# Kernel optimization log

Hardware: AMD Instinct MI355X
Metric: run time of the kernel (lower is better)

Reference implementation:

```python
import jax, jax.numpy as jnp
import numpy as np

LMAX, MMAX = 6, 2
C, COUT = 64, 64
E = 50000


def _perms():
    # l-primary coefficient order: for l in 0..lmax, m in -min(l,mmax)..min(l,mmax)
    lp = [(l, m) for l in range(LMAX + 1) for m in range(-min(l, MMAX), min(l, MMAX) + 1)]
    # m-primary order: m=0 block, then for each m>0: real (+m) block then imag (-m) block
    mp = [(l, 0) for l in range(LMAX + 1)]
    for m in range(1, MMAX + 1):
        mp += [(l, m) for l in range(m, LMAX + 1)]
        mp += [(l, -m) for l in range(m, LMAX + 1)]
    to_m = np.array([lp.index(p) for p in mp])   # gather: l-primary -> m-primary
    from_m = np.argsort(to_m)                    # inverse gather: m-primary -> l-primary
    return to_m, from_m

TO_M, FROM_M = _perms()


def setup_inputs() -> dict:
    key = jax.random.key(0)
    ks = jax.random.split(key, 6)
    sz0 = LMAX + 1                      # m_size[0] = 7
    in0 = sz0 * C                       # fc_m0 in_features = 448
    out0 = COUT * sz0                   # fc_m0 out_features = 448
    sz1, sz2 = LMAX, LMAX - 1           # m_size[1]=6, m_size[2]=5
    inp = {
        "x_embedding": jax.random.normal(ks[0], (E, len(TO_M), C), dtype=jnp.float32),
        "x_edge": jax.random.normal(ks[1], (E, 1), dtype=jnp.float32),
        "W0": jax.random.normal(ks[2], (out0, in0), dtype=jnp.float32) / np.sqrt(in0),
        "b0": jnp.zeros((out0,), dtype=jnp.float32),
        "W1": jax.random.normal(ks[3], (2 * COUT * sz1, sz1 * C), dtype=jnp.float32) / np.sqrt(2 * sz1 * C),
        "W2": jax.random.normal(ks[4], (2 * COUT * sz2, sz2 * C), dtype=jnp.float32) / np.sqrt(2 * sz2 * C),
    }
    return inp


def reference(x_embedding, x_edge, W0, b0, W1, W2):
    num_edges = x_embedding.shape[0]
    # _m_primary: permute coefficients to m-primary layout
    x = x_embedding[:, TO_M, :]                         # [E, 29, C]
    out = []
    # m = 0 path (fc_m0 with bias)
    sz0 = LMAX + 1
    x0 = x[:, :sz0, :].reshape(num_edges, sz0 * C)
    x0 = x0 @ W0.T + b0                                 # [E, sz0*COUT]
    out.append(x0.reshape(num_edges, sz0, COUT))
    # m = 1..mmax: SO2_m_Convolution (complex multiply structure)
    offset = sz0
    for m, Wm in zip(range(1, MMAX + 1), (W1, W2)):
        sz = LMAX - m + 1
        xm = x[:, offset:offset + 2 * sz, :].reshape(num_edges, 2, sz * C)
        y = jnp.einsum('enk,ok->eno', xm, Wm)           # [E, 2, 2*sz*COUT]
        half = sz * COUT
        x_r, x_i = y[..., :half], y[..., half:]
        x_m_r = x_r[:, 0:1] - x_i[:, 1:2]
        x_m_i = x_r[:, 1:2] + x_i[:, 0:1]
        xm_out = jnp.concatenate((x_m_r, x_m_i), axis=1)  # [E, 2, sz*COUT]
        out.append(xm_out.reshape(num_edges, 2 * sz, COUT))
        offset += 2 * sz
    out = jnp.concatenate(out, axis=1)                  # [E, 29, COUT] m-primary
    # _l_primary: back to l-primary layout
    return out[:, FROM_M, :]
```

## Files before the change

### kernel.cpp

```cpp
#include <hip/hip_runtime.h>
#include <hip/hip_bf16.h>

typedef __attribute__((ext_vector_type(8))) short short8;
typedef __attribute__((ext_vector_type(4))) float f32x4;

#define XSTRIDE 1856
#define CCH 64
#define OFF1 229376
#define OFF2 819200
#define WTOT 1228800

__constant__ int d_TO_M[29] = {0,2,6,11,16,21,26, 3,7,12,17,22,27, 1,5,10,15,20,25,
                               8,13,18,23,28, 4,9,14,19,24};

__device__ __forceinline__ short f2bf(float f) {
    __hip_bfloat16 h = __float2bfloat16(f);
    return __builtin_bit_cast(short, h);
}

__device__ __forceinline__ void load16_lds(const void* g, void* l) {
    __builtin_amdgcn_global_load_lds((const __attribute__((address_space(1))) unsigned int*)g,
                                     (__attribute__((address_space(3))) unsigned int*)l, 16, 0, 0);
}

__global__ __launch_bounds__(256) void prep_weights(const float* __restrict__ W0,
                                                    const float* __restrict__ W1,
                                                    const float* __restrict__ W2,
                                                    short* __restrict__ ws) {
    int idx = blockIdx.x * 256 + threadIdx.x;
    if (idx < OFF1) {
        ws[idx] = (idx < 448 * 448) ? f2bf(W0[idx]) : (short)0;
        return;
    }
    if (idx < OFF2) {
        int i = idx - OFF1;
        int n = i / 768, k = i % 768;
        int no = n / 384, ni = n % 384;
        int ki = k % 384;
        float v;
        if (no == (k / 384)) v =  W1[ni * 384 + ki];
        else if (no == 0)    v = -W1[(384 + ni) * 384 + ki];
        else                 v =  W1[(384 + ni) * 384 + ki];
        ws[idx] = f2bf(v);
        return;
    }
    if (idx < WTOT) {
        int i = idx - OFF2;
        int n = i / 640, k = i % 640;
        int no = n / 320, ni = n % 320;
        int ki = k % 320;
        float v;
        if (no == (k / 320)) v =  W2[ni * 320 + ki];
        else if (no == 0)    v = -W2[(320 + ni) * 320 + ki];
        else                 v =  W2[(320 + ni) * 320 + ki];
        ws[idx] = f2bf(v);
    }
}

__global__ __launch_bounds__(256, 2) void so2_gemm_f(const float* __restrict__ x,
                                                     const float* __restrict__ b0,
                                                     const short* __restrict__ wsW,
                                                     float* __restrict__ out,
                                                     int E, int nwg) {
    int orig = blockIdx.x;
    int q8 = nwg >> 3, r8 = nwg & 7;
    int xcd = orig & 7, pos = orig >> 3;
    int wgid = (xcd < r8 ? xcd * (q8 + 1) : r8 * (q8 + 1) + (xcd - r8) * q8) + pos;

    int etile = wgid / 15;
    int ncol  = wgid % 15;
    int blk, ntl;
    if (ncol < 4)       { blk = 0; ntl = ncol; }
    else if (ncol < 10) { blk = 1; ntl = ncol - 4; }
    else                { blk = 2; ntl = ncol - 10; }
    const int Kb     = (blk == 0) ? 448 : (blk == 1) ? 768 : 640;
    const int ksteps = Kb >> 5;
    const int kbase  = (blk == 0) ? 0 : (blk == 1) ? 7 : 19;
    const int nrows  = (blk == 0) ? 7 : (blk == 1) ? 12 : 10;
    const long woff  = (blk == 0) ? 0 : (blk == 1) ? (long)OFF1 : (long)OFF2;
    const short* Wb  = wsW + woff;
    const int n0 = ntl * 128;

    __shared__ float Af[3][128 * 32];
    __shared__ short Bf[2][128 * 32];

    const int tid  = threadIdx.x;
    const int w    = tid >> 6, lane = tid & 63;
    const int wr   = w >> 1,   wc   = w & 1;
    const int lrow = lane & 15, lk  = lane >> 4;
    const int ebase = etile * 128;

    const int lr = lane >> 3;
    const int ca = (lane & 7) ^ lr;
    const int rbq = lane >> 2;
    const int cb = (lane & 3) ^ ((lane >> 3) & 3);

    f32x4 acc[4][4] = {};

    auto stageA = [&](int kt, int pb) {
        int g = d_TO_M[kbase + (kt >> 1)];
        const float* src = x + (size_t)g * CCH + (kt & 1) * 32 + ca * 4;
#pragma unroll
        for (int j = 0; j < 4; ++j) {
            int rb = w * 32 + j * 8;
            int e = ebase + rb + lr;
            if (e >= E) e = E - 1;
            load16_lds(src + (size_t)e * XSTRIDE,
                       (char*)&Af[pb][rb * 32] + lane * 16);
        }
    };
    auto stageB = [&](int kt, int pb) {
        const short* src = Wb + (size_t)kt * 32 + cb * 8;
#pragma unroll
        for (int j = 0; j < 2; ++j) {
            int rb = w * 32 + j * 16;
            int n = n0 + rb + rbq;
            load16_lds(src + (size_t)n * Kb,
                       (char*)&Bf[pb][rb * 32] + lane * 16);
        }
    };
    auto compute = [&](int pa, int pbb) {
        short8 af[4], bf[4];
#pragma unroll
        for (int mf = 0; mf < 4; ++mf) {
            int r = wr * 64 + mf * 16 + lrow;
            int s0 = (2 * lk) ^ (lrow & 7);
            int s1 = (2 * lk + 1) ^ (lrow & 7);
            f32x4 lo = *(const f32x4*)&Af[pa][r * 32 + s0 * 4];
            f32x4 hi = *(const f32x4*)&Af[pa][r * 32 + s1 * 4];
            short8 v;
#pragma unroll
            for (int j = 0; j < 4; ++j) { v[j] = f2bf(lo[j]); v[4 + j] = f2bf(hi[j]); }
            af[mf] = v;
        }
#pragma unroll
        for (int nf = 0; nf < 4; ++nf) {
            int r = wc * 64 + nf * 16 + lrow;
            int s = lk ^ ((lrow >> 1) & 3);
            bf[nf] = *(const short8*)&Bf[pbb][r * 32 + s * 8];
        }
#pragma unroll
        for (int mf = 0; mf < 4; ++mf)
#pragma unroll
            for (int nf = 0; nf < 4; ++nf)
                acc[mf][nf] = __builtin_amdgcn_mfma_f32_16x16x32_bf16(af[mf], bf[nf], acc[mf][nf], 0, 0, 0);
    };

    stageA(0, 0);
    stageB(0, 0);
    stageA(1, 1);
    asm volatile("s_waitcnt vmcnt(4)" ::: "memory");
    __builtin_amdgcn_s_barrier();
    __builtin_amdgcn_sched_barrier(0);

    int pa = 0;
    for (int kt = 0; kt < ksteps; ++kt) {
        int pa1 = pa + 1; if (pa1 == 3) pa1 = 0;
        int pa2 = pa1 + 1; if (pa2 == 3) pa2 = 0;
        if (kt + 1 < ksteps) stageB(kt + 1, (kt + 1) & 1);
        __builtin_amdgcn_sched_barrier(0);
        if (kt + 2 < ksteps) stageA(kt + 2, pa2);
        compute(pa, kt & 1);
        if (kt + 2 < ksteps) {
            asm volatile("s_waitcnt vmcnt(4)" ::: "memory");
        } else if (kt + 1 < ksteps) {
            asm volatile("s_waitcnt vmcnt(0)" ::: "memory");
        }
        __builtin_amdgcn_s_barrier();
        __builtin_amdgcn_sched_barrier(0);
        pa = pa1;
    }

    int mrow_l = ntl * 2 + wc;
    if (mrow_l < nrows) {
        int lp = d_TO_M[kbase + mrow_l];
        float* op = out + (size_t)lp * CCH;
#pragma unroll
        for (int nf = 0; nf < 4; ++nf) {
            int c = nf * 16 + lrow;
            float bias = 0.f;
            if (blk == 0) bias = b0[mrow_l * 64 + c];
#pragma unroll
            for (int mf = 0; mf < 4; ++mf) {
                int e0 = ebase + wr * 64 + mf * 16 + lk * 4;
#pragma unroll
                for (int j = 0; j < 4; ++j) {
                    int e = e0 + j;
                    if (e < E) op[(size_t)e * XSTRIDE + c] = acc[mf][nf][j] + bias;
                }
            }
        }
    }
}

extern "C" void kernel_launch(void* const* d_in, const int* in_sizes, int n_in,
                              void* d_out, int out_size, void* d_ws, size_t ws_size,
                              hipStream_t stream) {
    const float* x_emb = (const float*)d_in[0];
    const float* W0 = (const float*)d_in[2];
    const float* b0 = (const float*)d_in[3];
    const float* W1 = (const float*)d_in[4];
    const float* W2 = (const float*)d_in[5];
    float* out = (float*)d_out;
    short* ws  = (short*)d_ws;

    const int E = in_sizes[0] / (29 * CCH);
    const int etiles = (E + 127) / 128;
    const int nwg = etiles * 15;

    prep_weights<<<(WTOT + 255) / 256, 256, 0, stream>>>(W0, W1, W2, ws);
    so2_gemm_f<<<nwg, 256, 0, stream>>>(x_emb, b0, (const short*)ws, out, E, nwg);
}
```

Before: 452.7 us.

## Keep weight stripe resident in LDS and stream activations directly from global

Replaces the pipelined 128x128 tiled GEMM with a kernel where each 512-thread block loads one 64-column weight stripe (the full K) into LDS once, then loops over four 512-edge groups. Activations are read straight from global memory into registers and converted to bf16, with no LDS staging or double buffering. The aim is to stop re-fetching weights for every edge tile and to drop the barrier-heavy multi-stage pipeline. In exchange, A loads are no longer software-pipelined, and each stripe re-reads the same activation rows across the 29 stripes, so activation reuse now relies on cache.

Result: slower. 662.4 us (+46.3%).

```diff
diff --git a/kernel.cpp b/kernel.cpp
--- a/kernel.cpp
+++ b/kernel.cpp
@@ -3,6 +3,7 @@
 
 typedef __attribute__((ext_vector_type(8))) short short8;
 typedef __attribute__((ext_vector_type(4))) float f32x4;
+typedef __attribute__((ext_vector_type(4))) unsigned int uint4v;
 
 #define XSTRIDE 1856
 #define CCH 64
@@ -10,17 +11,9 @@
 #define OFF2 819200
 #define WTOT 1228800
 
-__constant__ int d_TO_M[29] = {0,2,6,11,16,21,26, 3,7,12,17,22,27, 1,5,10,15,20,25,
-                               8,13,18,23,28, 4,9,14,19,24};
-
 __device__ __forceinline__ short f2bf(float f) {
     __hip_bfloat16 h = __float2bfloat16(f);
     return __builtin_bit_cast(short, h);
-}
-
-__device__ __forceinline__ void load16_lds(const void* g, void* l) {
-    __builtin_amdgcn_global_load_lds((const __attribute__((address_space(1))) unsigned int*)g,
-                                     (__attribute__((address_space(3))) unsigned int*)l, 16, 0, 0);
 }
 
 __global__ __launch_bounds__(256) void prep_weights(const float* __restrict__ W0,
@@ -57,140 +50,122 @@
     }
 }
 
-__global__ __launch_bounds__(256, 2) void so2_gemm_f(const float* __restrict__ x,
-                                                     const float* __restrict__ b0,
-                                                     const short* __restrict__ wsW,
-                                                     float* __restrict__ out,
-                                                     int E, int nwg) {
-    int orig = blockIdx.x;
-    int q8 = nwg >> 3, r8 = nwg & 7;
-    int xcd = orig & 7, pos = orig >> 3;
-    int wgid = (xcd < r8 ? xcd * (q8 + 1) : r8 * (q8 + 1) + (xcd - r8) * q8) + pos;
+template<int FAM>
+__device__ __forceinline__ void run_family(short* __restrict__ Bl, int stripe_g, int eg4,
+                                           const float* __restrict__ x,
+                                           const float* __restrict__ b0,
+                                           const short* __restrict__ wsW,
+                                           float* __restrict__ out, int E) {
+    constexpr int KB    = FAM == 0 ? 448 : FAM == 1 ? 768 : 640;
+    constexpr int NGR   = KB / 64;
+    constexpr int KBASE = FAM == 0 ? 0 : FAM == 1 ? 7 : 19;
+    constexpr long WOFF = FAM == 0 ? 0 : FAM == 1 ? (long)OFF1 : (long)OFF2;
+    constexpr int LSTR  = KB + 8;
+    constexpr int KB8   = KB / 8;
+    constexpr int TOM[29] = {0,2,6,11,16,21,26, 3,7,12,17,22,27, 1,5,10,15,20,25,
+                             8,13,18,23,28, 4,9,14,19,24};
+    const int sl = stripe_g - KBASE;
+    const int n0 = sl * 64;
+    const int tid = threadIdx.x;
 
-    int etile = wgid / 15;
-    int ncol  = wgid % 15;
-    int blk, ntl;
-    if (ncol < 4)       { blk = 0; ntl = ncol; }
-    else if (ncol < 10) { blk = 1; ntl = ncol - 4; }
-    else                { blk = 2; ntl = ncol - 10; }
-    const int Kb     = (blk == 0) ? 448 : (blk == 1) ? 768 : 640;
-    const int ksteps = Kb >> 5;
-    const int kbase  = (blk == 0) ? 0 : (blk == 1) ? 7 : 19;
-    const int nrows  = (blk == 0) ? 7 : (blk == 1) ? 12 : 10;
-    const long woff  = (blk == 0) ? 0 : (blk == 1) ? (long)OFF1 : (long)OFF2;
-    const short* Wb  = wsW + woff;
-    const int n0 = ntl * 128;
+    const short* Wb = wsW + WOFF + (size_t)n0 * KB;
+#pragma unroll
+    for (int it = 0; it < NGR; ++it) {
+        int flat = it * 512 + tid;
+        int n = flat / KB8, kc = flat % KB8;
+        *(uint4v*)&Bl[n * LSTR + kc * 8] = *(const uint4v*)(Wb + (size_t)n * KB + kc * 8);
+    }
+    __syncthreads();
 
-    __shared__ float Af[3][128 * 32];
-    __shared__ short Bf[2][128 * 32];
+    const int w = tid >> 6, lane = tid & 63;
+    const int lrow = lane & 15, lk = lane >> 4;
+    const int lp = TOM[stripe_g];
 
-    const int tid  = threadIdx.x;
-    const int w    = tid >> 6, lane = tid & 63;
-    const int wr   = w >> 1,   wc   = w & 1;
-    const int lrow = lane & 15, lk  = lane >> 4;
-    const int ebase = etile * 128;
+    int bbase[4];
+#pragma unroll
+    for (int nf = 0; nf < 4; ++nf) bbase[nf] = (nf * 16 + lrow) * LSTR + lk * 8;
 
-    const int lr = lane >> 3;
-    const int ca = (lane & 7) ^ lr;
-    const int rbq = lane >> 2;
-    const int cb = (lane & 3) ^ ((lane >> 3) & 3);
+    float bias[4] = {0.f, 0.f, 0.f, 0.f};
+    if (FAM == 0) {
+#pragma unroll
+        for (int nf = 0; nf < 4; ++nf) bias[nf] = b0[n0 + nf * 16 + lrow];
+    }
 
-    f32x4 acc[4][4] = {};
+    for (int eo = 0; eo < 4; ++eo) {
+        int egroup = eg4 * 4 + eo;
+        if (egroup * 512 >= E) break;
+        const int eb = egroup * 512 + w * 64;
 
-    auto stageA = [&](int kt, int pb) {
-        int g = d_TO_M[kbase + (kt >> 1)];
-        const float* src = x + (size_t)g * CCH + (kt & 1) * 32 + ca * 4;
-#pragma unroll
-        for (int j = 0; j < 4; ++j) {
-            int rb = w * 32 + j * 8;
-            int e = ebase + rb + lr;
-            if (e >= E) e = E - 1;
-            load16_lds(src + (size_t)e * XSTRIDE,
-                       (char*)&Af[pb][rb * 32] + lane * 16);
-        }
-    };
-    auto stageB = [&](int kt, int pb) {
-        const short* src = Wb + (size_t)kt * 32 + cb * 8;
-#pragma unroll
-        for (int j = 0; j < 2; ++j) {
-            int rb = w * 32 + j * 16;
-            int n = n0 + rb + rbq;
-            load16_lds(src + (size_t)n * Kb,
-                       (char*)&Bf[pb][rb * 32] + lane * 16);
-        }
-    };
-    auto compute = [&](int pa, int pbb) {
-        short8 af[4], bf[4];
+        const float* pa[4];
 #pragma unroll
         for (int mf = 0; mf < 4; ++mf) {
-            int r = wr * 64 + mf * 16 + lrow;
-            int s0 = (2 * lk) ^ (lrow & 7);
-            int s1 = (2 * lk + 1) ^ (lrow & 7);
-            f32x4 lo = *(const f32x4*)&Af[pa][r * 32 + s0 * 4];
-            f32x4 hi = *(const f32x4*)&Af[pa][r * 32 + s1 * 4];
-            short8 v;
+            int e = eb + mf * 16 + lrow;
+            if (e >= E) e = E - 1;
+            pa[mf] = x + (size_t)e * XSTRIDE + lk * 8;
+        }
+
+        f32x4 acc[4][4] = {};
 #pragma unroll
-            for (int j = 0; j < 4; ++j) { v[j] = f2bf(lo[j]); v[4 + j] = f2bf(hi[j]); }
-            af[mf] = v;
+        for (int gi = 0; gi < NGR; ++gi) {
+            const int g = TOM[KBASE + gi];
+#pragma unroll
+            for (int ks = 0; ks < 2; ++ks) {
+                short8 af[4], bf[4];
+#pragma unroll
+                for (int mf = 0; mf < 4; ++mf) {
+                    f32x4 lo = *(const f32x4*)(pa[mf] + g * 64 + ks * 32);
+                    f32x4 hi = *(const f32x4*)(pa[mf] + g * 64 + ks * 32 + 4);
+                    short8 v;
+#pragma unroll
+                    for (int j = 0; j < 4; ++j) { v[j] = f2bf(lo[j]); v[4 + j] = f2bf(hi[j]); }
+                    af[mf] = v;
+                }
+#pragma unroll
+                for (int nf = 0; nf < 4; ++nf)
+                    bf[nf] = *(const short8*)&Bl[bbase[nf] + gi * 64 + ks * 32];
+#pragma unroll
+                for (int mf = 0; mf < 4; ++mf)
+#pragma unroll
+                    for (int nf = 0; nf < 4; ++nf)
+                        acc[mf][nf] = __builtin_amdgcn_mfma_f32_16x16x32_bf16(af[mf], bf[nf], acc[mf][nf], 0, 0, 0);
+            }
         }
+
 #pragma unroll
-        for (int nf = 0; nf < 4; ++nf) {
-            int r = wc * 64 + nf * 16 + lrow;
-            int s = lk ^ ((lrow >> 1) & 3);
-            bf[nf] = *(const short8*)&Bf[pbb][r * 32 + s * 8];
-        }
+        for (int mf = 0; mf < 4; ++mf) {
 #pragma unroll
-        for (int mf = 0; mf < 4; ++mf)
+            for (int j = 0; j < 4; ++j) {
+                int e = eb + mf * 16 + lk * 4 + j;
+                if (e < E) {
+                    float* op = out + (size_t)e * XSTRIDE + lp * 64 + lrow;
 #pragma unroll
-            for (int nf = 0; nf < 4; ++nf)
-                acc[mf][nf] = __builtin_amdgcn_mfma_f32_16x16x32_bf16(af[mf], bf[nf], acc[mf][nf], 0, 0, 0);
-    };
-
-    stageA(0, 0);
-    stageB(0, 0);
-    stageA(1, 1);
-    asm volatile("s_waitcnt vmcnt(4)" ::: "memory");
-    __builtin_amdgcn_s_barrier();
-    __builtin_amdgcn_sched_barrier(0);
-
-    int pa = 0;
-    for (int kt = 0; kt < ksteps; ++kt) {
-        int pa1 = pa + 1; if (pa1 == 3) pa1 = 0;
-        int pa2 = pa1 + 1; if (pa2 == 3) pa2 = 0;
-        if (kt + 1 < ksteps) stageB(kt + 1, (kt + 1) & 1);
-        __builtin_amdgcn_sched_barrier(0);
-        if (kt + 2 < ksteps) stageA(kt + 2, pa2);
-        compute(pa, kt & 1);
-        if (kt + 2 < ksteps) {
-            asm volatile("s_waitcnt vmcnt(4)" ::: "memory");
-        } else if (kt + 1 < ksteps) {
-            asm volatile("s_waitcnt vmcnt(0)" ::: "memory");
-        }
-        __builtin_amdgcn_s_barrier();
-        __builtin_amdgcn_sched_barrier(0);
-        pa = pa1;
-    }
-
-    int mrow_l = ntl * 2 + wc;
-    if (mrow_l < nrows) {
-        int lp = d_TO_M[kbase + mrow_l];
-        float* op = out + (size_t)lp * CCH;
-#pragma unroll
-        for (int nf = 0; nf < 4; ++nf) {
-            int c = nf * 16 + lrow;
-            float bias = 0.f;
-            if (blk == 0) bias = b0[mrow_l * 64 + c];
-#pragma unroll
-            for (int mf = 0; mf < 4; ++mf) {
-                int e0 = ebase + wr * 64 + mf * 16 + lk * 4;
-#pragma unroll
-                for (int j = 0; j < 4; ++j) {
-                    int e = e0 + j;
-                    if (e < E) op[(size_t)e * XSTRIDE + c] = acc[mf][nf][j] + bias;
+                    for (int nf = 0; nf < 4; ++nf)
+                        op[nf * 16] = acc[mf][nf][j] + bias[nf];
                 }
             }
         }
     }
+}
+
+__global__ __launch_bounds__(512) void so2_bres(const float* __restrict__ x,
+                                                const float* __restrict__ b0,
+                                                const short* __restrict__ wsW,
+                                                float* __restrict__ out,
+                                                int E, int nb) {
+    __shared__ short Bl[64 * 776];
+
+    int bid = blockIdx.x;
+    int q = nb >> 3, r = nb & 7;
+    int xcd = bid & 7, pos = bid >> 3;
+    int cnt = q + (xcd < r ? 1 : 0);
+    if (pos >= cnt) return;
+    int base = (xcd < r) ? xcd * (q + 1) : r * (q + 1) + (xcd - r) * q;
+    int wgid = base + pos;
+
+    int eg4 = wgid / 29, stripe = wgid % 29;
+    if (stripe < 7)       run_family<0>(Bl, stripe, eg4, x, b0, wsW, out, E);
+    else if (stripe < 19) run_family<1>(Bl, stripe, eg4, x, b0, wsW, out, E);
+    else                  run_family<2>(Bl, stripe, eg4, x, b0, wsW, out, E);
 }
 
 extern "C" void kernel_launch(void* const* d_in, const int* in_sizes, int n_in,
@@ -205,9 +180,11 @@
     short* ws  = (short*)d_ws;
 
     const int E = in_sizes[0] / (29 * CCH);
-    const int etiles = (E + 127) / 128;
-    const int nwg = etiles * 15;
+    const int neg  = (E + 511) / 512;
+    const int eg4c = (neg + 3) / 4;
+    const int nb   = 29 * eg4c;
+    const int grid = ((nb + 7) / 8) * 8;
 
     prep_weights<<<(WTOT + 255) / 256, 256, 0, stream>>>(W0, W1, W2, ws);
-    so2_gemm_f<<<nwg, 256, 0, stream>>>(x_emb, b0, (const short*)ws, out, E, nwg);
+    so2_bres<<<grid, 512, 0, stream>>>(x_emb, b0, (const short*)ws, out, E, nb);
 }
```
